# Optimization experiments

Hardware: AMD Instinct MI355X
Metric: run time of the kernel (lower is better)

The kernel has to match this reference:

```python
import jax, jax.numpy as jnp
import numpy as np

B, S, H = 256, 1, 2048
Q_SIZE = 4096        # num_heads * head_dim = 32 * 128
QKV = 4 * H          # expected_linear_qkv = 8192
K_SZ = 4             # conv kernel size
C = 32               # ssm channels
WSCALE = 0.02


def setup_inputs() -> dict:
    key = jax.random.key(0)
    ks = jax.random.split(key, 13)
    return {
        "hidden_states": jax.random.normal(ks[0], (B, S, H), jnp.float32),
        "W_qkv": jax.random.normal(ks[1], (QKV, H), jnp.float32) * WSCALE,
        "b_qkv": jax.random.normal(ks[2], (QKV,), jnp.float32) * WSCALE,
        "W_gate": jax.random.normal(ks[3], (2 * H, H), jnp.float32) * WSCALE,
        "W_alpha": jax.random.normal(ks[4], (C, H), jnp.float32) * WSCALE,
        "W_beta": jax.random.normal(ks[5], (C, H), jnp.float32) * WSCALE,
        "W_out": jax.random.normal(ks[6], (H, 2 * H), jnp.float32) * WSCALE,
        "ssm_state_a": jax.random.normal(ks[7], (C,), jnp.float32),
        "ssm_dt_bias": jax.random.normal(ks[8], (C,), jnp.float32),
        "ssm_norm_weight": jnp.ones((128,), jnp.float32),
        "conv_kernel": jax.random.normal(ks[9], (QKV, K_SZ), jnp.float32) * WSCALE,
        "ssm_state": jax.random.normal(ks[10], (B, C), jnp.float32),
        "conv_state": jax.random.normal(ks[11], (B, K_SZ, QKV), jnp.float32),
    }


def reference(hidden_states, W_qkv, b_qkv, W_gate, W_alpha, W_beta, W_out,
              ssm_state_a, ssm_dt_bias, ssm_norm_weight, conv_kernel,
              ssm_state, conv_state):
    bsz = hidden_states.shape[0]
    # qkv projection (decode: only last token matters downstream)
    qkv = jnp.einsum('bsh,dh->bsd', hidden_states, W_qkv) + b_qkv  # [B,S,4H]
    mixed_qkv = qkv[:, -1, :].astype(jnp.float32)                  # [B,4H]
    hidden_last = hidden_states[:, -1, :]                          # [B,H]

    # roll conv state and append current token, then causal conv1d step
    cs = jnp.concatenate([conv_state[:, 1:, :], mixed_qkv[:, None, :]], axis=1)  # [B,K,4H]
    conv_out = jnp.einsum('bkd,dk->bd', cs, conv_kernel)           # [B,4H]

    target_size = conv_out.shape[-1] - Q_SIZE                      # 2H = 4096
    k_size = target_size // 2                                      # 2048
    core_base = conv_out[:, Q_SIZE:]                               # [B,2H]
    k_proj = core_base[:, :k_size]
    v_proj = core_base[:, k_size:]

    # alpha/beta gating of the SSM state
    a = hidden_last @ W_alpha.T                                    # [B,C]
    b = hidden_last @ W_beta.T                                     # [B,C]
    g = -jnp.exp(ssm_state_a)[None, :] * jax.nn.softplus(a + ssm_dt_bias[None, :])
    beta = jax.nn.sigmoid(b)

    group_width = k_size // C                                      # 64
    v_group = v_proj[:, :group_width * C].reshape(bsz, C, group_width).mean(-1)
    k_group = k_proj[:, :group_width * C].reshape(bsz, C, group_width).mean(-1)

    new_state = jnp.exp(g) * ssm_state + beta * v_group            # [B,C]
    state_signal = new_state * jax.nn.sigmoid(k_group)             # [B,C]

    repeat_factor = target_size // C                               # 128
    expanded = jnp.repeat(state_signal, repeat_factor, axis=-1)[:, :target_size]

    core = core_base + expanded
    core = core * jax.lax.rsqrt(jnp.mean(core * core, axis=-1, keepdims=True) + 1e-6)
    gate = jax.nn.sigmoid(hidden_last @ W_gate.T).astype(jnp.float32)
    core = core * gate * jnp.mean(ssm_norm_weight)
    core = core.astype(hidden_states.dtype)

    out = (core @ W_out.T)[:, None, :]                             # [B,1,H]
    return out
```

## Files before the change

kernel.cpp:

```cpp
#include <hip/hip_runtime.h>
#include <hip/hip_bf16.h>
#include <stdint.h>

#define BSZ 256
#define NQ 4096
#define N1 8320
#define K1 2048
#define N3 2048
#define K3 4096

typedef __attribute__((ext_vector_type(8))) short bf16x8;
typedef __attribute__((ext_vector_type(4))) float f32x4;

__device__ __forceinline__ unsigned short f2bf(float f) {
  union { float f; unsigned u; } v; v.f = f;
  unsigned r = v.u + 0x7fffu + ((v.u >> 16) & 1u);
  return (unsigned short)(r >> 16);
}

__device__ __forceinline__ bf16x8 pack8(float4 a, float4 b) {
  union { bf16x8 v; unsigned short u[8]; } o;
  o.u[0] = f2bf(a.x); o.u[1] = f2bf(a.y); o.u[2] = f2bf(a.z); o.u[3] = f2bf(a.w);
  o.u[4] = f2bf(b.x); o.u[5] = f2bf(b.y); o.u[6] = f2bf(b.z); o.u[7] = f2bf(b.w);
  return o.v;
}

__device__ __forceinline__ void barrier_lgkm_only() {
  asm volatile("s_waitcnt lgkmcnt(0)" ::: "memory");
  asm volatile("s_barrier" ::: "memory");
}

__global__ __launch_bounds__(256) void cvt_kernel(const float* __restrict__ x,
                                                  unsigned short* __restrict__ y) {
  int i = (blockIdx.x * 256 + threadIdx.x) * 8;
  float4 a = *(const float4*)(x + i);
  float4 b = *(const float4*)(x + i + 4);
  ushort4 o0 = { f2bf(a.x), f2bf(a.y), f2bf(a.z), f2bf(a.w) };
  ushort4 o1 = { f2bf(b.x), f2bf(b.y), f2bf(b.z), f2bf(b.w) };
  *(ushort4*)(y + i) = o0;
  *(ushort4*)(y + i + 4) = o1;
}


__global__ __launch_bounds__(256, 4) void gemm1_kernel(
    const unsigned short* __restrict__ A16,
    const float* __restrict__ Wqkv, const float* __restrict__ Wgate,
    const float* __restrict__ Walpha, const float* __restrict__ Wbeta,
    float* __restrict__ P) {
  __shared__ __align__(16) char sA[2][8192];
  __shared__ __align__(16) char sB[2][2112];
  const int tid = threadIdx.x, lane = tid & 63, wv = tid >> 6;
  const int wr = wv >> 1, wc = wv & 1, l15 = lane & 15, q = lane >> 4;
  const int rt = blockIdx.x * 128;
  const int n0 = blockIdx.y * 32;
  const int kb = blockIdx.z * 1024;

  const int am = tid >> 1, ah = tid & 1;
  const char* pA = (const char*)(A16 + (size_t)(rt + am) * K1 + kb) + ah * 32;
  const int axor = (am >> 3) & 3;
  const int aoff0 = (((2 * ah) ^ axor) * 2048) + am * 16;
  const int aoff1 = (((2 * ah + 1) ^ axor) * 2048) + am * 16;

  const bool doB = (tid < 128);
  const int bn = tid >> 2, bp = tid & 3;
  const float* pB = Walpha;
  if (doB) {
    int ng = n0 + bn;
    const float* base;
    if (ng < 4096)       base = Wqkv  + (size_t)(4096 + ng) * K1;
    else if (ng < 8192)  base = Wgate + (size_t)(ng - 4096) * K1;
    else if (ng < 8224)  base = Walpha + (size_t)(ng - 8192) * K1;
    else if (ng < 8256)  base = Wbeta + (size_t)(ng - 8224) * K1;
    else                 base = Walpha;
    pB = base + kb + bp * 8;
  }
  const int boff = ((bp ^ (bn & 3)) * 528) + bn * 16;

  const int nr = wc * 16 + l15;
  const int cboff = ((q ^ (nr & 3)) * 528) + nr * 16;
  int caoff[4];
#pragma unroll
  for (int i = 0; i < 4; i++) {
    int m = wr * 64 + i * 16 + l15;
    caoff[i] = ((q ^ ((m >> 3) & 3)) * 2048) + m * 16;
  }

  f32x4 acc[4];
#pragma unroll
  for (int i = 0; i < 4; i++) { f32x4 z = {0.f, 0.f, 0.f, 0.f}; acc[i] = z; }

  uint4 a0 = *(const uint4*)pA;
  uint4 a1 = *(const uint4*)(pA + 16);
  float4 b0, b1;
  if (doB) { b0 = *(const float4*)pB; b1 = *(const float4*)(pB + 4); }

  for (int it = 0; it < 32; it++) {
    char* sAb = sA[it & 1]; char* sBb = sB[it & 1];
    *(uint4*)(sAb + aoff0) = a0;
    *(uint4*)(sAb + aoff1) = a1;
    if (doB) *(bf16x8*)(sBb + boff) = pack8(b0, b1);
    if (it + 1 < 32) {
      pA += 64;
      a0 = *(const uint4*)pA;
      a1 = *(const uint4*)(pA + 16);
      if (doB) { pB += 32; b0 = *(const float4*)pB; b1 = *(const float4*)(pB + 4); }
    }
    barrier_lgkm_only();
    bf16x8 bF = *(const bf16x8*)(sBb + cboff);
#pragma unroll
    for (int i = 0; i < 4; i++) {
      bf16x8 aF = *(const bf16x8*)(sAb + caoff[i]);
      acc[i] = __builtin_amdgcn_mfma_f32_16x16x32_bf16(aF, bF, acc[i], 0, 0, 0);
    }
  }

  float* Pz = P + (size_t)blockIdx.z * ((size_t)BSZ * N1);
#pragma unroll
  for (int i = 0; i < 4; i++) {
    int row = rt + wr * 64 + i * 16 + (lane >> 4) * 4;
    int col = n0 + wc * 16 + l15;
#pragma unroll
    for (int r = 0; r < 4; r++)
      Pz[(size_t)(row + r) * N1 + col] = acc[i][r];
  }
}

__global__ __launch_bounds__(1024) void fuse_kernel(
    const float* __restrict__ P,
    const float* __restrict__ bqkv,
    const float* __restrict__ ck,
    const float* __restrict__ cstate,
    const float* __restrict__ ssa,
    const float* __restrict__ dtb,
    const float* __restrict__ nw,
    const float* __restrict__ sstate,
    unsigned short* __restrict__ C16) {
  __shared__ float gsum[64];
  __shared__ float ssl[32];
  __shared__ float red[20];
  const int b = blockIdx.x, tid = threadIdx.x;
  const int lane = tid & 63, wv = tid >> 6;
  const float* P0 = P + (size_t)b * N1;
  const float* P1 = P + (size_t)(BSZ + b) * N1;
  const int j = tid * 4;

  float4 g0x = *(const float4*)(P0 + NQ + j);
  float4 g1x = *(const float4*)(P1 + NQ + j);

  if (wv == 0) {
    float m = nw[lane] + nw[lane + 64];
#pragma unroll
    for (int off = 32; off; off >>= 1) m += __shfl_down(m, off, 64);
    if (lane == 0) red[16] = m * (1.f / 128.f);
  }

  float4 q0 = *(const float4*)(P0 + j);
  float4 q1 = *(const float4*)(P1 + j);
  float4 bq = *(const float4*)(bqkv + NQ + j);
  float mqx = q0.x + q1.x + bq.x, mqy = q0.y + q1.y + bq.y;
  float mqz = q0.z + q1.z + bq.z, mqw = q0.w + q1.w + bq.w;
  const float* csb = cstate + (size_t)b * 4 * 8192 + NQ + j;
  float4 c1 = *(const float4*)(csb + 8192);
  float4 c2 = *(const float4*)(csb + 16384);
  float4 c3 = *(const float4*)(csb + 24576);
  float4 k0v = *(const float4*)(ck + (size_t)(NQ + j) * 4);
  float4 k1v = *(const float4*)(ck + (size_t)(NQ + j + 1) * 4);
  float4 k2v = *(const float4*)(ck + (size_t)(NQ + j + 2) * 4);
  float4 k3v = *(const float4*)(ck + (size_t)(NQ + j + 3) * 4);
  float4 cbv;
  cbv.x = c1.x * k0v.x + c2.x * k0v.y + c3.x * k0v.z + mqx * k0v.w;
  cbv.y = c1.y * k1v.x + c2.y * k1v.y + c3.y * k1v.z + mqy * k1v.w;
  cbv.z = c1.z * k2v.x + c2.z * k2v.y + c3.z * k2v.z + mqz * k2v.w;
  cbv.w = c1.w * k3v.x + c2.w * k3v.y + c3.w * k3v.z + mqw * k3v.w;
  {
    float s = cbv.x + cbv.y + cbv.z + cbv.w;
    s += __shfl_xor(s, 1, 64); s += __shfl_xor(s, 2, 64);
    s += __shfl_xor(s, 4, 64); s += __shfl_xor(s, 8, 64);
    if ((lane & 15) == 0) gsum[tid >> 4] = s;
  }
  __syncthreads();

  if (tid < 32) {
    float a  = P0[8192 + tid] + P1[8192 + tid];
    float bc = P0[8224 + tid] + P1[8224 + tid];
    float kg = gsum[tid] * (1.f / 64.f);
    float vg = gsum[32 + tid] * (1.f / 64.f);
    float x = a + dtb[tid];
    float sp = fmaxf(x, 0.f) + log1pf(expf(-fabsf(x)));
    float g = -expf(ssa[tid]) * sp;
    float beta = 1.f / (1.f + expf(-bc));
    float ns = expf(g) * sstate[b * 32 + tid] + beta * vg;
    ssl[tid] = ns / (1.f + expf(-kg));
  }
  __syncthreads();

  float sv = ssl[j >> 7];
  float4 v = cbv;
  v.x += sv; v.y += sv; v.z += sv; v.w += sv;
  float sq = v.x * v.x + v.y * v.y + v.z * v.z + v.w * v.w;
#pragma unroll
  for (int off = 32; off; off >>= 1) sq += __shfl_down(sq, off, 64);
  if (lane == 0) red[wv] = sq;
  __syncthreads();
  if (tid == 0) {
    float t = 0.f;
#pragma unroll
    for (int w = 0; w < 16; w++) t += red[w];
    red[17] = rsqrtf(t * (1.f / 4096.f) + 1e-6f);
  }
  __syncthreads();
  float rms = red[17], mwv = red[16];

  float ox = v.x * rms * mwv / (1.f + expf(-(g0x.x + g1x.x)));
  float oy = v.y * rms * mwv / (1.f + expf(-(g0x.y + g1x.y)));
  float oz = v.z * rms * mwv / (1.f + expf(-(g0x.z + g1x.z)));
  float ow = v.w * rms * mwv / (1.f + expf(-(g0x.w + g1x.w)));
  ushort4 u = { f2bf(ox), f2bf(oy), f2bf(oz), f2bf(ow) };
  *(ushort4*)(C16 + (size_t)b * 4096 + j) = u;
}

__global__ __launch_bounds__(256, 4) void gemm3_kernel(
    const unsigned short* __restrict__ A16,
    const float* __restrict__ Wout,
    float* __restrict__ OP) {
  __shared__ __align__(16) char sA[2][8192];
  __shared__ __align__(16) char sB[2][2112];
  const int tid = threadIdx.x, lane = tid & 63, wv = tid >> 6;
  const int wr = wv >> 1, wc = wv & 1, l15 = lane & 15, q = lane >> 4;
  const int rt = blockIdx.x * 128;
  const int n0 = blockIdx.y * 32;
  const int kb = blockIdx.z * 512;

  const int am = tid >> 1, ah = tid & 1;
  const char* pA = (const char*)(A16 + (size_t)(rt + am) * K3 + kb) + ah * 32;
  const int axor = (am >> 3) & 3;
  const int aoff0 = (((2 * ah) ^ axor) * 2048) + am * 16;
  const int aoff1 = (((2 * ah + 1) ^ axor) * 2048) + am * 16;

  const bool doB = (tid < 128);
  const int bn = tid >> 2, bp = tid & 3;
  const float* pB = Wout + (size_t)(n0 + bn) * K3 + kb + bp * 8;
  const int boff = ((bp ^ (bn & 3)) * 528) + bn * 16;

  const int nr = wc * 16 + l15;
  const int cboff = ((q ^ (nr & 3)) * 528) + nr * 16;
  int caoff[4];
#pragma unroll
  for (int i = 0; i < 4; i++) {
    int m = wr * 64 + i * 16 + l15;
    caoff[i] = ((q ^ ((m >> 3) & 3)) * 2048) + m * 16;
  }

  f32x4 acc[4];
#pragma unroll
  for (int i = 0; i < 4; i++) { f32x4 z = {0.f, 0.f, 0.f, 0.f}; acc[i] = z; }

  uint4 a0 = *(const uint4*)pA;
  uint4 a1 = *(const uint4*)(pA + 16);
  float4 b0, b1;
  if (doB) { b0 = *(const float4*)pB; b1 = *(const float4*)(pB + 4); }

  for (int it = 0; it < 16; it++) {
    char* sAb = sA[it & 1]; char* sBb = sB[it & 1];
    *(uint4*)(sAb + aoff0) = a0;
    *(uint4*)(sAb + aoff1) = a1;
    if (doB) *(bf16x8*)(sBb + boff) = pack8(b0, b1);
    if (it + 1 < 16) {
      pA += 64;
      a0 = *(const uint4*)pA;
      a1 = *(const uint4*)(pA + 16);
      if (doB) { pB += 32; b0 = *(const float4*)pB; b1 = *(const float4*)(pB + 4); }
    }
    barrier_lgkm_only();
    bf16x8 bF = *(const bf16x8*)(sBb + cboff);
#pragma unroll
    for (int i = 0; i < 4; i++) {
      bf16x8 aF = *(const bf16x8*)(sAb + caoff[i]);
      acc[i] = __builtin_amdgcn_mfma_f32_16x16x32_bf16(aF, bF, acc[i], 0, 0, 0);
    }
  }

  float* Oz = OP + (size_t)blockIdx.z * ((size_t)BSZ * N3);
#pragma unroll
  for (int i = 0; i < 4; i++) {
    int row = rt + wr * 64 + i * 16 + (lane >> 4) * 4;
    int col = n0 + wc * 16 + l15;
#pragma unroll
    for (int r = 0; r < 4; r++)
      Oz[(size_t)(row + r) * N3 + col] = acc[i][r];
  }
}

__global__ __launch_bounds__(256) void reduce_kernel(const float* __restrict__ OP,
                                                     float* __restrict__ out) {
  int i = (blockIdx.x * 256 + threadIdx.x) * 4;
  float4 s = *(const float4*)(OP + i);
#pragma unroll
  for (int z = 1; z < 8; z++) {
    float4 v = *(const float4*)(OP + (size_t)z * BSZ * N3 + i);
    s.x += v.x; s.y += v.y; s.z += v.z; s.w += v.w;
  }
  *(float4*)(out + i) = s;
}

extern "C" void kernel_launch(void* const* d_in, const int* in_sizes, int n_in,
                              void* d_out, int out_size, void* d_ws, size_t ws_size,
                              hipStream_t stream) {
  const float* hidden = (const float*)d_in[0];
  const float* Wqkv   = (const float*)d_in[1];
  const float* bqkv   = (const float*)d_in[2];
  const float* Wgate  = (const float*)d_in[3];
  const float* Walpha = (const float*)d_in[4];
  const float* Wbeta  = (const float*)d_in[5];
  const float* Wout   = (const float*)d_in[6];
  const float* ssa    = (const float*)d_in[7];
  const float* dtb    = (const float*)d_in[8];
  const float* nw     = (const float*)d_in[9];
  const float* ck     = (const float*)d_in[10];
  const float* sstate = (const float*)d_in[11];
  const float* cstate = (const float*)d_in[12];
  float* out = (float*)d_out;

  char* ws = (char*)d_ws;
  unsigned short* A16 = (unsigned short*)ws;
  float* P   = (float*)(ws + (1 << 20));
  unsigned short* C16 = (unsigned short*)(ws + (1 << 20) + 17039360);
  float* OP  = (float*)(ws + (1 << 20) + 17039360 + (2 << 20));

  cvt_kernel<<<256, 256, 0, stream>>>(hidden, A16);
  gemm1_kernel<<<dim3(2, 260, 2), 256, 0, stream>>>(A16, Wqkv, Wgate, Walpha, Wbeta, P);
  fuse_kernel<<<256, 1024, 0, stream>>>(P, bqkv, ck, cstate, ssa, dtb, nw, sstate, C16);
  gemm3_kernel<<<dim3(2, 64, 8), 256, 0, stream>>>(C16, Wout, OP);
  reduce_kernel<<<512, 256, 0, stream>>>(OP, out);
}
```

Measured before the change: 253.0 us.

## Restructure GEMMs as register-resident split-K with atomic accumulation, drop reduce kernel

```diff
diff --git a/kernel.cpp b/kernel.cpp
--- a/kernel.cpp
+++ b/kernel.cpp
@@ -4,8 +4,8 @@
 
 #define BSZ 256
 #define NQ 4096
-#define N1 8320
 #define K1 2048
+#define N1P 8448
 #define N3 2048
 #define K3 4096
 
@@ -23,11 +23,6 @@
   o.u[0] = f2bf(a.x); o.u[1] = f2bf(a.y); o.u[2] = f2bf(a.z); o.u[3] = f2bf(a.w);
   o.u[4] = f2bf(b.x); o.u[5] = f2bf(b.y); o.u[6] = f2bf(b.z); o.u[7] = f2bf(b.w);
   return o.v;
-}
-
-__device__ __forceinline__ void barrier_lgkm_only() {
-  asm volatile("s_waitcnt lgkmcnt(0)" ::: "memory");
-  asm volatile("s_barrier" ::: "memory");
 }
 
 __global__ __launch_bounds__(256) void cvt_kernel(const float* __restrict__ x,
@@ -41,87 +36,79 @@
   *(ushort4*)(y + i + 4) = o1;
 }
 
-
-__global__ __launch_bounds__(256, 4) void gemm1_kernel(
+__device__ __forceinline__ const float* brow1(int col, const float* Wqkv, const float* Wgate,
+                                              const float* Wa, const float* Wb) {
+  if (col < 4096) return Wqkv + (size_t)(4096 + col) * K1;
+  if (col < 8192) return Wgate + (size_t)(col - 4096) * K1;
+  if (col < 8224) return Wa + (size_t)(col - 8192) * K1;
+  if (col < 8256) return Wb + (size_t)(col - 8224) * K1;
+  return Wa;
+}
+
+__global__ __launch_bounds__(512) void gemm1_kernel(
     const unsigned short* __restrict__ A16,
     const float* __restrict__ Wqkv, const float* __restrict__ Wgate,
     const float* __restrict__ Walpha, const float* __restrict__ Wbeta,
     float* __restrict__ P) {
-  __shared__ __align__(16) char sA[2][8192];
-  __shared__ __align__(16) char sB[2][2112];
   const int tid = threadIdx.x, lane = tid & 63, wv = tid >> 6;
-  const int wr = wv >> 1, wc = wv & 1, l15 = lane & 15, q = lane >> 4;
-  const int rt = blockIdx.x * 128;
-  const int n0 = blockIdx.y * 32;
-  const int kb = blockIdx.z * 1024;
-
-  const int am = tid >> 1, ah = tid & 1;
-  const char* pA = (const char*)(A16 + (size_t)(rt + am) * K1 + kb) + ah * 32;
-  const int axor = (am >> 3) & 3;
-  const int aoff0 = (((2 * ah) ^ axor) * 2048) + am * 16;
-  const int aoff1 = (((2 * ah + 1) ^ axor) * 2048) + am * 16;
-
-  const bool doB = (tid < 128);
-  const int bn = tid >> 2, bp = tid & 3;
-  const float* pB = Walpha;
-  if (doB) {
-    int ng = n0 + bn;
-    const float* base;
-    if (ng < 4096)       base = Wqkv  + (size_t)(4096 + ng) * K1;
-    else if (ng < 8192)  base = Wgate + (size_t)(ng - 4096) * K1;
-    else if (ng < 8224)  base = Walpha + (size_t)(ng - 8192) * K1;
-    else if (ng < 8256)  base = Wbeta + (size_t)(ng - 8224) * K1;
-    else                 base = Walpha;
-    pB = base + kb + bp * 8;
-  }
-  const int boff = ((bp ^ (bn & 3)) * 528) + bn * 16;
-
-  const int nr = wc * 16 + l15;
-  const int cboff = ((q ^ (nr & 3)) * 528) + nr * 16;
-  int caoff[4];
-#pragma unroll
-  for (int i = 0; i < 4; i++) {
-    int m = wr * 64 + i * 16 + l15;
-    caoff[i] = ((q ^ ((m >> 3) & 3)) * 2048) + m * 16;
-  }
-
-  f32x4 acc[4];
-#pragma unroll
-  for (int i = 0; i < 4; i++) { f32x4 z = {0.f, 0.f, 0.f, 0.f}; acc[i] = z; }
-
-  uint4 a0 = *(const uint4*)pA;
-  uint4 a1 = *(const uint4*)(pA + 16);
-  float4 b0, b1;
-  if (doB) { b0 = *(const float4*)pB; b1 = *(const float4*)(pB + 4); }
-
-  for (int it = 0; it < 32; it++) {
-    char* sAb = sA[it & 1]; char* sBb = sB[it & 1];
-    *(uint4*)(sAb + aoff0) = a0;
-    *(uint4*)(sAb + aoff1) = a1;
-    if (doB) *(bf16x8*)(sBb + boff) = pack8(b0, b1);
-    if (it + 1 < 32) {
-      pA += 64;
-      a0 = *(const uint4*)pA;
-      a1 = *(const uint4*)(pA + 16);
-      if (doB) { pB += 32; b0 = *(const float4*)pB; b1 = *(const float4*)(pB + 4); }
-    }
-    barrier_lgkm_only();
-    bf16x8 bF = *(const bf16x8*)(sBb + cboff);
-#pragma unroll
-    for (int i = 0; i < 4; i++) {
-      bf16x8 aF = *(const bf16x8*)(sAb + caoff[i]);
-      acc[i] = __builtin_amdgcn_mfma_f32_16x16x32_bf16(aF, bF, acc[i], 0, 0, 0);
-    }
-  }
-
-  float* Pz = P + (size_t)blockIdx.z * ((size_t)BSZ * N1);
-#pragma unroll
-  for (int i = 0; i < 4; i++) {
-    int row = rt + wr * 64 + i * 16 + (lane >> 4) * 4;
-    int col = n0 + wc * 16 + l15;
-#pragma unroll
-    for (int r = 0; r < 4; r++)
-      Pz[(size_t)(row + r) * N1 + col] = acc[i][r];
+  const int wm = wv >> 1, wc = wv & 1;
+  const int l15 = lane & 15, q = lane >> 4;
+  const int nbase = blockIdx.x * 264;
+  const int kb = blockIdx.y * 256;
+
+  float4 bst[8][2];
+  {
+    int col = nbase + wc * 16 + l15;
+    const float* bp = brow1(col, Wqkv, Wgate, Walpha, Wbeta) + kb + q * 8;
+#pragma unroll
+    for (int ks = 0; ks < 8; ks++) {
+      bst[ks][0] = *(const float4*)(bp + ks * 32);
+      bst[ks][1] = *(const float4*)(bp + ks * 32 + 4);
+    }
+  }
+
+  bf16x8 aF[4][8];
+  {
+    const unsigned short* aBase = A16 + (size_t)(wm * 64 + l15) * K1 + kb + q * 8;
+#pragma unroll
+    for (int i = 0; i < 4; i++)
+#pragma unroll
+      for (int ks = 0; ks < 8; ks++)
+        aF[i][ks] = *(const bf16x8*)(aBase + (size_t)i * 16 * K1 + ks * 32);
+  }
+
+#pragma unroll 1
+  for (int s = 0; s < 9; s++) {
+    f32x4 acc[4];
+#pragma unroll
+    for (int i = 0; i < 4; i++) { f32x4 z = {0.f, 0.f, 0.f, 0.f}; acc[i] = z; }
+#pragma unroll
+    for (int ks = 0; ks < 8; ks++) {
+      bf16x8 bF = pack8(bst[ks][0], bst[ks][1]);
+#pragma unroll
+      for (int i = 0; i < 4; i++)
+        acc[i] = __builtin_amdgcn_mfma_f32_16x16x32_bf16(aF[i][ks], bF, acc[i], 0, 0, 0);
+    }
+    if (s + 1 < 9) {
+      int col = nbase + (s + 1) * 32 + wc * 16 + l15;
+      const float* bp = brow1(col, Wqkv, Wgate, Walpha, Wbeta) + kb + q * 8;
+#pragma unroll
+      for (int ks = 0; ks < 8; ks++) {
+        bst[ks][0] = *(const float4*)(bp + ks * 32);
+        bst[ks][1] = *(const float4*)(bp + ks * 32 + 4);
+      }
+    }
+    int lcol = s * 32 + wc * 16 + l15;
+    if (lcol < 264) {
+      int col = nbase + lcol;
+#pragma unroll
+      for (int i = 0; i < 4; i++) {
+        int row = wm * 64 + i * 16 + q * 4;
+#pragma unroll
+        for (int r = 0; r < 4; r++)
+          atomicAdd(&P[(size_t)(row + r) * N1P + col], acc[i][r]);
+      }
+    }
   }
 }
 
@@ -140,12 +127,10 @@
   __shared__ float red[20];
   const int b = blockIdx.x, tid = threadIdx.x;
   const int lane = tid & 63, wv = tid >> 6;
-  const float* P0 = P + (size_t)b * N1;
-  const float* P1 = P + (size_t)(BSZ + b) * N1;
+  const float* Pb = P + (size_t)b * N1P;
   const int j = tid * 4;
 
-  float4 g0x = *(const float4*)(P0 + NQ + j);
-  float4 g1x = *(const float4*)(P1 + NQ + j);
+  float4 gx = *(const float4*)(Pb + NQ + j);
 
   if (wv == 0) {
     float m = nw[lane] + nw[lane + 64];
@@ -154,11 +139,9 @@
     if (lane == 0) red[16] = m * (1.f / 128.f);
   }
 
-  float4 q0 = *(const float4*)(P0 + j);
-  float4 q1 = *(const float4*)(P1 + j);
+  float4 qv = *(const float4*)(Pb + j);
   float4 bq = *(const float4*)(bqkv + NQ + j);
-  float mqx = q0.x + q1.x + bq.x, mqy = q0.y + q1.y + bq.y;
-  float mqz = q0.z + q1.z + bq.z, mqw = q0.w + q1.w + bq.w;
+  float mqx = qv.x + bq.x, mqy = qv.y + bq.y, mqz = qv.z + bq.z, mqw = qv.w + bq.w;
   const float* csb = cstate + (size_t)b * 4 * 8192 + NQ + j;
   float4 c1 = *(const float4*)(csb + 8192);
   float4 c2 = *(const float4*)(csb + 16384);
@@ -181,8 +164,8 @@
   __syncthreads();
 
   if (tid < 32) {
-    float a  = P0[8192 + tid] + P1[8192 + tid];
-    float bc = P0[8224 + tid] + P1[8224 + tid];
+    float a  = Pb[8192 + tid];
+    float bc = Pb[8224 + tid];
     float kg = gsum[tid] * (1.f / 64.f);
     float vg = gsum[32 + tid] * (1.f / 64.f);
     float x = a + dtb[tid];
@@ -211,96 +194,73 @@
   __syncthreads();
   float rms = red[17], mwv = red[16];
 
-  float ox = v.x * rms * mwv / (1.f + expf(-(g0x.x + g1x.x)));
-  float oy = v.y * rms * mwv / (1.f + expf(-(g0x.y + g1x.y)));
-  float oz = v.z * rms * mwv / (1.f + expf(-(g0x.z + g1x.z)));
-  float ow = v.w * rms * mwv / (1.f + expf(-(g0x.w + g1x.w)));
+  float ox = v.x * rms * mwv / (1.f + expf(-gx.x));
+  float oy = v.y * rms * mwv / (1.f + expf(-gx.y));
+  float oz = v.z * rms * mwv / (1.f + expf(-gx.z));
+  float ow = v.w * rms * mwv / (1.f + expf(-gx.w));
   ushort4 u = { f2bf(ox), f2bf(oy), f2bf(oz), f2bf(ow) };
   *(ushort4*)(C16 + (size_t)b * 4096 + j) = u;
 }
 
-__global__ __launch_bounds__(256, 4) void gemm3_kernel(
-    const unsigned short* __restrict__ A16,
+__global__ __launch_bounds__(512) void gemm3_kernel(
+    const unsigned short* __restrict__ C16,
     const float* __restrict__ Wout,
-    float* __restrict__ OP) {
-  __shared__ __align__(16) char sA[2][8192];
-  __shared__ __align__(16) char sB[2][2112];
+    float* __restrict__ out) {
   const int tid = threadIdx.x, lane = tid & 63, wv = tid >> 6;
-  const int wr = wv >> 1, wc = wv & 1, l15 = lane & 15, q = lane >> 4;
-  const int rt = blockIdx.x * 128;
-  const int n0 = blockIdx.y * 32;
-  const int kb = blockIdx.z * 512;
-
-  const int am = tid >> 1, ah = tid & 1;
-  const char* pA = (const char*)(A16 + (size_t)(rt + am) * K3 + kb) + ah * 32;
-  const int axor = (am >> 3) & 3;
-  const int aoff0 = (((2 * ah) ^ axor) * 2048) + am * 16;
-  const int aoff1 = (((2 * ah + 1) ^ axor) * 2048) + am * 16;
-
-  const bool doB = (tid < 128);
-  const int bn = tid >> 2, bp = tid & 3;
-  const float* pB = Wout + (size_t)(n0 + bn) * K3 + kb + bp * 8;
-  const int boff = ((bp ^ (bn & 3)) * 528) + bn * 16;
-
-  const int nr = wc * 16 + l15;
-  const int cboff = ((q ^ (nr & 3)) * 528) + nr * 16;
-  int caoff[4];
-#pragma unroll
-  for (int i = 0; i < 4; i++) {
-    int m = wr * 64 + i * 16 + l15;
-    caoff[i] = ((q ^ ((m >> 3) & 3)) * 2048) + m * 16;
-  }
-
-  f32x4 acc[4];
-#pragma unroll
-  for (int i = 0; i < 4; i++) { f32x4 z = {0.f, 0.f, 0.f, 0.f}; acc[i] = z; }
-
-  uint4 a0 = *(const uint4*)pA;
-  uint4 a1 = *(const uint4*)(pA + 16);
-  float4 b0, b1;
-  if (doB) { b0 = *(const float4*)pB; b1 = *(const float4*)(pB + 4); }
-
-  for (int it = 0; it < 16; it++) {
-    char* sAb = sA[it & 1]; char* sBb = sB[it & 1];
-    *(uint4*)(sAb + aoff0) = a0;
-    *(uint4*)(sAb + aoff1) = a1;
-    if (doB) *(bf16x8*)(sBb + boff) = pack8(b0, b1);
-    if (it + 1 < 16) {
-      pA += 64;
-      a0 = *(const uint4*)pA;
-      a1 = *(const uint4*)(pA + 16);
-      if (doB) { pB += 32; b0 = *(const float4*)pB; b1 = *(const float4*)(pB + 4); }
-    }
-    barrier_lgkm_only();
-    bf16x8 bF = *(const bf16x8*)(sBb + cboff);
+  const int wm = wv >> 1, wc = wv & 1;
+  const int l15 = lane & 15, q = lane >> 4;
+  const int nbase = blockIdx.x * 256;
+  const int kb = blockIdx.y * 128;
+
+  float4 bst[4][2];
+  {
+    const float* bp = Wout + (size_t)(nbase + wc * 16 + l15) * K3 + kb + q * 8;
+#pragma unroll
+    for (int ks = 0; ks < 4; ks++) {
+      bst[ks][0] = *(const float4*)(bp + ks * 32);
+      bst[ks][1] = *(const float4*)(bp + ks * 32 + 4);
+    }
+  }
+
+  bf16x8 aF[4][4];
+  {
+    const unsigned short* aBase = C16 + (size_t)(wm * 64 + l15) * K3 + kb + q * 8;
+#pragma unroll
+    for (int i = 0; i < 4; i++)
+#pragma unroll
+      for (int ks = 0; ks < 4; ks++)
+        aF[i][ks] = *(const bf16x8*)(aBase + (size_t)i * 16 * K3 + ks * 32);
+  }
+
+#pragma unroll 1
+  for (int s = 0; s < 8; s++) {
+    f32x4 acc[4];
+#pragma unroll
+    for (int i = 0; i < 4; i++) { f32x4 z = {0.f, 0.f, 0.f, 0.f}; acc[i] = z; }
+#pragma unroll
+    for (int ks = 0; ks < 4; ks++) {
+      bf16x8 bF = pack8(bst[ks][0], bst[ks][1]);
+#pragma unroll
+      for (int i = 0; i < 4; i++)
+        acc[i] = __builtin_amdgcn_mfma_f32_16x16x32_bf16(aF[i][ks], bF, acc[i], 0, 0, 0);
+    }
+    if (s + 1 < 8) {
+      const float* bp = Wout + (size_t)(nbase + (s + 1) * 32 + wc * 16 + l15) * K3 + kb + q * 8;
+#pragma unroll
+      for (int ks = 0; ks < 4; ks++) {
+        bst[ks][0] = *(const float4*)(bp + ks * 32);
+        bst[ks][1] = *(const float4*)(bp + ks * 32 + 4);
+      }
+    }
+    int col = nbase + s * 32 + wc * 16 + l15;
 #pragma unroll
     for (int i = 0; i < 4; i++) {
-      bf16x8 aF = *(const bf16x8*)(sAb + caoff[i]);
-      acc[i] = __builtin_amdgcn_mfma_f32_16x16x32_bf16(aF, bF, acc[i], 0, 0, 0);
-    }
-  }
-
-  float* Oz = OP + (size_t)blockIdx.z * ((size_t)BSZ * N3);
-#pragma unroll
-  for (int i = 0; i < 4; i++) {
-    int row = rt + wr * 64 + i * 16 + (lane >> 4) * 4;
-    int col = n0 + wc * 16 + l15;
-#pragma unroll
-    for (int r = 0; r < 4; r++)
-      Oz[(size_t)(row + r) * N3 + col] = acc[i][r];
-  }
-}
-
-__global__ __launch_bounds__(256) void reduce_kernel(const float* __restrict__ OP,
-                                                     float* __restrict__ out) {
-  int i = (blockIdx.x * 256 + threadIdx.x) * 4;
-  float4 s = *(const float4*)(OP + i);
-#pragma unroll
-  for (int z = 1; z < 8; z++) {
-    float4 v = *(const float4*)(OP + (size_t)z * BSZ * N3 + i);
-    s.x += v.x; s.y += v.y; s.z += v.z; s.w += v.w;
-  }
-  *(float4*)(out + i) = s;
+      int row = wm * 64 + i * 16 + q * 4;
+#pragma unroll
+      for (int r = 0; r < 4; r++)
+        atomicAdd(&out[(size_t)(row + r) * N3 + col], acc[i][r]);
+    }
+  }
 }
 
 extern "C" void kernel_launch(void* const* d_in, const int* in_sizes, int n_in,
@@ -323,13 +283,13 @@
 
   char* ws = (char*)d_ws;
   unsigned short* A16 = (unsigned short*)ws;
-  float* P   = (float*)(ws + (1 << 20));
-  unsigned short* C16 = (unsigned short*)(ws + (1 << 20) + 17039360);
-  float* OP  = (float*)(ws + (1 << 20) + 17039360 + (2 << 20));
-
+  float* P = (float*)(ws + (1 << 20));
+  unsigned short* C16 = (unsigned short*)(ws + (1 << 20) + 8650752);
+
+  hipMemsetAsync(P, 0, (size_t)BSZ * N1P * sizeof(float), stream);
+  hipMemsetAsync(out, 0, (size_t)BSZ * N3 * sizeof(float), stream);
   cvt_kernel<<<256, 256, 0, stream>>>(hidden, A16);
-  gemm1_kernel<<<dim3(2, 260, 2), 256, 0, stream>>>(A16, Wqkv, Wgate, Walpha, Wbeta, P);
+  gemm1_kernel<<<dim3(32, 8), 512, 0, stream>>>(A16, Wqkv, Wgate, Walpha, Wbeta, P);
   fuse_kernel<<<256, 1024, 0, stream>>>(P, bqkv, ck, cstate, ssa, dtb, nw, sstate, C16);
-  gemm3_kernel<<<dim3(2, 64, 8), 256, 0, stream>>>(C16, Wout, OP);
-  reduce_kernel<<<512, 256, 0, stream>>>(OP, out);
-}
+  gemm3_kernel<<<dim3(8, 32), 512, 0, stream>>>(C16, Wout, out);
+}
```

Result: slower. 317.4 us (+25.5%).
